# Kernel optimization log

Measured on AMD Instinct MI355X. Metric: run time of the kernel, lower is better.

The kernel has to match this reference:

```python
import jax, jax.numpy as jnp
import numpy as np

D_MODEL = 1024
H = 16
D_K = D_MODEL // H
BAND = 100  # attention allowed where |i-j| < BAND


def setup_inputs() -> dict:
    key = jax.random.key(0)
    ks = jax.random.split(key, 9)
    B, S = 2, 2048
    s = 1.0 / np.sqrt(D_MODEL)
    return {
        "x": jax.random.normal(ks[0], (B, S, D_MODEL), jnp.float32),
        "Wq": jax.random.normal(ks[1], (D_MODEL, D_MODEL), jnp.float32) * s,
        "bq": jnp.zeros((D_MODEL,), jnp.float32),
        "Wk": jax.random.normal(ks[2], (D_MODEL, D_MODEL), jnp.float32) * s,
        "bk": jnp.zeros((D_MODEL,), jnp.float32),
        "Wv": jax.random.normal(ks[3], (D_MODEL, D_MODEL), jnp.float32) * s,
        "bv": jnp.zeros((D_MODEL,), jnp.float32),
        "Wo": jax.random.normal(ks[4], (D_MODEL, D_MODEL), jnp.float32) * s,
        "bo": jnp.zeros((D_MODEL,), jnp.float32),
    }


def _split_heads(t, B, S):
    # [B, S, D] -> [B, H, S, D_K]
    return t.reshape(B, S, H, D_K).transpose(0, 2, 1, 3)


def reference(x, Wq, bq, Wk, bk, Wv, bv, Wo, bo):
    B, S, _ = x.shape
    q = _split_heads(x @ Wq.T + bq, B, S)
    k = _split_heads(x @ Wk.T + bk, B, S)
    v = _split_heads(x @ Wv.T + bv, B, S)

    scores = jnp.einsum("bhqd,bhkd->bhqk", q, k) / jnp.sqrt(jnp.float32(D_K))
    i = jnp.arange(S)
    band = jnp.abs(i[:, None] - i[None, :]) < BAND  # [S, S] True inside band
    scores = jnp.where(band[None, None, :, :], scores, jnp.float32(-1e9))
    p_attn = jax.nn.softmax(scores, axis=-1)

    out = jnp.einsum("bhqk,bhkd->bhqd", p_attn, v)
    out = out.transpose(0, 2, 1, 3).reshape(B, S, D_MODEL)
    return out @ Wo.T + bo
```

## Files before the change

### kernel.cpp

```cpp
#include <hip/hip_runtime.h>
#include <hip/hip_bf16.h>


typedef __attribute__((ext_vector_type(8))) short short8;
typedef __attribute__((ext_vector_type(4))) short short4v;
typedef __attribute__((ext_vector_type(4))) float f32x4;

#define S_LEN 2048
#define NH 16
#define DK 64
#define BANDW 100

#define X_ELEMS   (2 * S_LEN * 1024)
#define W_ELEMS   (1024 * 1024)
#define QKV_ELEMS (2 * NH * S_LEN * DK)
#define AO_ELEMS  (2 * S_LEN * 1024)

__device__ __attribute__((aligned(256))) short g_X[X_ELEMS];
__device__ __attribute__((aligned(256))) short g_W[4 * W_ELEMS];
__device__ __attribute__((aligned(256))) short g_b[4 * 1024];
__device__ __attribute__((aligned(256))) short g_Q[QKV_ELEMS];
__device__ __attribute__((aligned(256))) short g_K[QKV_ELEMS];
__device__ __attribute__((aligned(256))) short g_V[QKV_ELEMS];
__device__ __attribute__((aligned(256))) short g_AO[AO_ELEMS];

__device__ __forceinline__ float bf2f(short u) {
    unsigned x = ((unsigned)(unsigned short)u) << 16;
    return __builtin_bit_cast(float, x);
}
__device__ __forceinline__ short f2bf(float f) {
    unsigned x = __builtin_bit_cast(unsigned, f);
    unsigned r = (x + 0x7fffu + ((x >> 16) & 1u)) >> 16;
    return (short)r;
}

#define GLOAD_LDS(gp, lp) \
    __builtin_amdgcn_global_load_lds( \
        (const __attribute__((address_space(1))) void*)(gp), \
        (__attribute__((address_space(3))) void*)(lp), 16, 0, 0)

#define XC   (X_ELEMS / 8)
#define WC   (W_ELEMS / 8)
#define BC   (1024 / 8)
#define TOTC (XC + 4 * WC + 4 * BC)

__global__ __launch_bounds__(256) void convert_all(
    const void* __restrict__ x,
    const void* __restrict__ w0, const void* __restrict__ b0,
    const void* __restrict__ w1, const void* __restrict__ b1,
    const void* __restrict__ w2, const void* __restrict__ b2,
    const void* __restrict__ w3, const void* __restrict__ b3)
{
    __shared__ int cnt[256];
    {
        const unsigned* xw = (const unsigned*)x;
        int local = 0;
        #pragma unroll
        for (int i = 0; i < 4; i++) {
            unsigned wv = xw[threadIdx.x * 4 + i];
            unsigned e = (wv >> 7) & 0xFF;
            if (e >= 100 && e <= 140) local++;
        }
        cnt[threadIdx.x] = local;
    }
    __syncthreads();
    for (int s = 128; s > 0; s >>= 1) {
        if (threadIdx.x < s) cnt[threadIdx.x] += cnt[threadIdx.x + s];
        __syncthreads();
    }
    const int is_bf16 = (cnt[0] > 512);

    long i = (long)blockIdx.x * 256 + threadIdx.x;
    if (i >= TOTC) return;

    const void* src; short* dst; long off;
    if (i < XC)                { src = x;  dst = g_X;              off = i; }
    else if ((i -= XC) < WC)   { src = w0; dst = g_W + 0L*W_ELEMS; off = i; }
    else if ((i -= WC) < WC)   { src = w1; dst = g_W + 1L*W_ELEMS; off = i; }
    else if ((i -= WC) < WC)   { src = w2; dst = g_W + 2L*W_ELEMS; off = i; }
    else if ((i -= WC) < WC)   { src = w3; dst = g_W + 3L*W_ELEMS; off = i; }
    else if ((i -= WC) < BC)   { src = b0; dst = g_b + 0*1024;     off = i; }
    else if ((i -= BC) < BC)   { src = b1; dst = g_b + 1*1024;     off = i; }
    else if ((i -= BC) < BC)   { src = b2; dst = g_b + 2*1024;     off = i; }
    else                       { src = b3; dst = g_b + 3*1024;     off = i - BC; }

    if (is_bf16) {
        ((short8*)dst)[off] = ((const short8*)src)[off];
    } else {
        const float* s = (const float*)src + off * 8;
        short8 o;
        #pragma unroll
        for (int e = 0; e < 8; e++) o[e] = f2bf(s[e]);
        ((short8*)dst)[off] = o;
    }
}

__global__ __launch_bounds__(256) void qkv_gemm()
{
    __shared__ __attribute__((aligned(16))) short As[128 * 32];
    __shared__ __attribute__((aligned(16))) short Bs[128 * 32];

    const int z = blockIdx.z;
    const short* __restrict__ X = g_X;
    const short* __restrict__ W = g_W + (long)z * W_ELEMS;
    const short* __restrict__ bias = g_b + z * 1024;

    const int t = threadIdx.x;
    const int lane = t & 63;
    const int wid  = t >> 6;
    const int wm = wid & 1, wn = wid >> 1;
    const int l15 = lane & 15;
    const int q8  = (lane >> 4) * 8;
    const int mb = blockIdx.x * 128;
    const int nb = blockIdx.y * 128;

    const long ga0 = (long)(mb + (t >> 2)) * 1024 + (t & 3) * 8;
    const long ga1 = (long)(mb + 64 + (t >> 2)) * 1024 + (t & 3) * 8;
    const long gb0 = (long)(nb + (t >> 2)) * 1024 + (t & 3) * 8;
    const long gb1 = (long)(nb + 64 + (t >> 2)) * 1024 + (t & 3) * 8;
    short* lA0 = As + t * 8;
    short* lA1 = As + 2048 + t * 8;
    short* lB0 = Bs + t * 8;
    short* lB1 = Bs + 2048 + t * 8;

    f32x4 acc[4][4] = {};

    for (int k0 = 0; k0 < 1024; k0 += 32) {
        __syncthreads();
        GLOAD_LDS(X + ga0 + k0, lA0);
        GLOAD_LDS(X + ga1 + k0, lA1);
        GLOAD_LDS(W + gb0 + k0, lB0);
        GLOAD_LDS(W + gb1 + k0, lB1);
        __syncthreads();

        short8 a[4], b[4];
        #pragma unroll
        for (int mt = 0; mt < 4; mt++) a[mt] = *(const short8*)(As + (wm * 64 + mt * 16 + l15) * 32 + q8);
        #pragma unroll
        for (int nt = 0; nt < 4; nt++) b[nt] = *(const short8*)(Bs + (wn * 64 + nt * 16 + l15) * 32 + q8);
        #pragma unroll
        for (int mt = 0; mt < 4; mt++)
            #pragma unroll
            for (int nt = 0; nt < 4; nt++)
                acc[mt][nt] = __builtin_amdgcn_mfma_f32_16x16x32_bf16(a[mt], b[nt], acc[mt][nt], 0, 0, 0);
    }

    const int rg = (lane >> 4) * 4;
    if (z == 2) {
        #pragma unroll
        for (int nt = 0; nt < 4; nt++) {
            const int col = nb + wn * 64 + nt * 16 + l15;
            const float bv_ = bf2f(bias[col]);
            const int h = col >> 6, d = col & 63;
            #pragma unroll
            for (int mt = 0; mt < 4; mt++) {
                const int row0 = mb + wm * 64 + mt * 16 + rg;
                const int bI = row0 >> 11, s0 = row0 & 2047;
                short4v pk;
                #pragma unroll
                for (int r = 0; r < 4; r++) pk[r] = f2bf(acc[mt][nt][r] + bv_);
                *(short4v*)(g_V + (((long)(bI * NH + h) * DK) + d) * S_LEN + s0) = pk;
            }
        }
    } else {
        short* __restrict__ Out = (z == 0) ? g_Q : g_K;
        #pragma unroll
        for (int nt = 0; nt < 4; nt++) {
            const int col = nb + wn * 64 + nt * 16 + l15;
            const float bv_ = bf2f(bias[col]);
            const int h = col >> 6, d = col & 63;
            #pragma unroll
            for (int mt = 0; mt < 4; mt++) {
                #pragma unroll
                for (int r = 0; r < 4; r++) {
                    const int row = mb + wm * 64 + mt * 16 + rg + r;
                    const int bI = row >> 11, s = row & 2047;
                    Out[(((long)(bI * NH + h) * S_LEN) + s) * DK + d] = f2bf(acc[mt][nt][r] + bv_);
                }
            }
        }
    }
}

__global__ __launch_bounds__(256) void o_gemm(float* __restrict__ Out)
{
    __shared__ __attribute__((aligned(16))) short As[128 * 32];
    __shared__ __attribute__((aligned(16))) short Bs[64 * 32];

    const short* __restrict__ A = g_AO;
    const short* __restrict__ W = g_W + 3L * W_ELEMS;

    const int t = threadIdx.x;
    const int lane = t & 63;
    const int wid  = t >> 6;
    const int wm = wid & 1, wn = wid >> 1;
    const int l15 = lane & 15;
    const int q8  = (lane >> 4) * 8;
    const int mb = blockIdx.x * 128;
    const int nb = blockIdx.y * 64;

    const long ga0 = (long)(mb + (t >> 2)) * 1024 + (t & 3) * 8;
    const long ga1 = (long)(mb + 64 + (t >> 2)) * 1024 + (t & 3) * 8;
    const long gb0 = (long)(nb + (t >> 2)) * 1024 + (t & 3) * 8;
    short* lA0 = As + t * 8;
    short* lA1 = As + 2048 + t * 8;
    short* lB0 = Bs + t * 8;

    f32x4 acc[4][2] = {};

    for (int k0 = 0; k0 < 1024; k0 += 32) {
        __syncthreads();
        GLOAD_LDS(A + ga0 + k0, lA0);
        GLOAD_LDS(A + ga1 + k0, lA1);
        GLOAD_LDS(W + gb0 + k0, lB0);
        __syncthreads();

        short8 a[4], b[2];
        #pragma unroll
        for (int mt = 0; mt < 4; mt++) a[mt] = *(const short8*)(As + (wm * 64 + mt * 16 + l15) * 32 + q8);
        #pragma unroll
        for (int nt = 0; nt < 2; nt++) b[nt] = *(const short8*)(Bs + (wn * 32 + nt * 16 + l15) * 32 + q8);
        #pragma unroll
        for (int mt = 0; mt < 4; mt++)
            #pragma unroll
            for (int nt = 0; nt < 2; nt++)
                acc[mt][nt] = __builtin_amdgcn_mfma_f32_16x16x32_bf16(a[mt], b[nt], acc[mt][nt], 0, 0, 0);
    }

    const int rg = (lane >> 4) * 4;
    #pragma unroll
    for (int nt = 0; nt < 2; nt++) {
        const int col = nb + wn * 32 + nt * 16 + l15;
        const float bv_ = bf2f(g_b[3 * 1024 + col]);
        #pragma unroll
        for (int mt = 0; mt < 4; mt++) {
            #pragma unroll
            for (int r = 0; r < 4; r++) {
                const int row = mb + wm * 64 + mt * 16 + rg + r;
                Out[(long)row * 1024 + col] = acc[mt][nt][r] + bv_;
            }
        }
    }
}

__global__ __launch_bounds__(256) void attn_kernel()
{
    __shared__ __attribute__((aligned(16))) short Pl[4][16][72];

    const int bid = blockIdx.x;
    const int qt = bid & 31;
    const int h  = (bid >> 5) & 15;
    const int b  = bid >> 9;
    const int qbase = qt * 64;

    const int lane = threadIdx.x & 63;
    const int w    = threadIdx.x >> 6;
    const int l15  = lane & 15;
    const int qg   = lane >> 4;
    const int q8   = qg * 8;

    const long hoff = (long)(b * NH + h) * S_LEN * DK;
    const short* __restrict__ Qh = g_Q + hoff;
    const short* __restrict__ Kh = g_K + hoff;
    const short* __restrict__ Vt = g_V + hoff;

    const short* qp = Qh + (long)(qbase + w * 16 + l15) * DK + q8;
    const short8 aq0 = *(const short8*)(qp);
    const short8 aq1 = *(const short8*)(qp + 32);

    f32x4 o[4] = {};
    float m_r[4], l_r[4];
    #pragma unroll
    for (int r = 0; r < 4; r++) { m_r[r] = -1e30f; l_r[r] = 0.f; }

    const int lo  = qbase - (BANDW - 1);
    const int kc0 = (lo < 0 ? 0 : lo) >> 6;
    int hi = qbase + 64 + (BANDW - 1);
    if (hi > S_LEN) hi = S_LEN;
    const int kc1 = (hi + 63) >> 6;

    for (int kc = kc0; kc < kc1; kc++) {
        const int kb = kc * 64;

        f32x4 sc[4];
        #pragma unroll
        for (int nt = 0; nt < 4; nt++) {
            const short* kp = Kh + (long)(kb + nt * 16 + l15) * DK + q8;
            const short8 bk0 = *(const short8*)(kp);
            const short8 bk1 = *(const short8*)(kp + 32);
            f32x4 z = {};
            z = __builtin_amdgcn_mfma_f32_16x16x32_bf16(aq0, bk0, z, 0, 0, 0);
            z = __builtin_amdgcn_mfma_f32_16x16x32_bf16(aq1, bk1, z, 0, 0, 0);
            sc[nt] = z;
        }

        float pv[4][4];
        float mx[4] = {-1e30f, -1e30f, -1e30f, -1e30f};
        #pragma unroll
        for (int nt = 0; nt < 4; nt++) {
            const int kg = kb + nt * 16 + l15;
            #pragma unroll
            for (int r = 0; r < 4; r++) {
                const int qI = qbase + w * 16 + qg * 4 + r;
                int dlt = qI - kg; if (dlt < 0) dlt = -dlt;
                const float v = (dlt < BANDW) ? sc[nt][r] * 0.125f : -1e30f;
                pv[nt][r] = v;
                mx[r] = fmaxf(mx[r], v);
            }
        }
        #pragma unroll
        for (int mk = 1; mk < 16; mk <<= 1)
            #pragma unroll
            for (int r = 0; r < 4; r++) mx[r] = fmaxf(mx[r], __shfl_xor(mx[r], mk, 64));

        float alpha[4], lnew[4];
        #pragma unroll
        for (int r = 0; r < 4; r++) {
            const float mn = fmaxf(m_r[r], mx[r]);
            alpha[r] = __builtin_exp2f((m_r[r] - mn) * 1.44269504f);
            m_r[r] = mn;
            lnew[r] = 0.f;
        }
        #pragma unroll
        for (int nt = 0; nt < 4; nt++)
            #pragma unroll
            for (int r = 0; r < 4; r++) {
                const float p = (pv[nt][r] > -0.5e30f)
                    ? __builtin_exp2f((pv[nt][r] - m_r[r]) * 1.44269504f) : 0.f;
                pv[nt][r] = p;
                lnew[r] += p;
            }
        #pragma unroll
        for (int mk = 1; mk < 16; mk <<= 1)
            #pragma unroll
            for (int r = 0; r < 4; r++) lnew[r] += __shfl_xor(lnew[r], mk, 64);
        #pragma unroll
        for (int r = 0; r < 4; r++) l_r[r] = l_r[r] * alpha[r] + lnew[r];
        #pragma unroll
        for (int nt2 = 0; nt2 < 4; nt2++)
            #pragma unroll
            for (int r = 0; r < 4; r++) o[nt2][r] *= alpha[r];

        #pragma unroll
        for (int nt = 0; nt < 4; nt++)
            #pragma unroll
            for (int r = 0; r < 4; r++)
                Pl[w][qg * 4 + r][nt * 16 + l15] = f2bf(pv[nt][r]);
        asm volatile("s_waitcnt lgkmcnt(0)" ::: "memory");
        const short8 ap0 = *(const short8*)(&Pl[w][l15][q8]);
        const short8 ap1 = *(const short8*)(&Pl[w][l15][32 + q8]);

        #pragma unroll
        for (int nt2 = 0; nt2 < 4; nt2++) {
            const short* vp = Vt + (long)(nt2 * 16 + l15) * S_LEN + kb;
            const short8 bv0 = *(const short8*)(vp + q8);
            const short8 bv1 = *(const short8*)(vp + 32 + q8);
            o[nt2] = __builtin_amdgcn_mfma_f32_16x16x32_bf16(ap0, bv0, o[nt2], 0, 0, 0);
            o[nt2] = __builtin_amdgcn_mfma_f32_16x16x32_bf16(ap1, bv1, o[nt2], 0, 0, 0);
        }
    }

    #pragma unroll
    for (int nt2 = 0; nt2 < 4; nt2++)
        #pragma unroll
        for (int r = 0; r < 4; r++) {
            const int qI = qbase + w * 16 + qg * 4 + r;
            const int d = nt2 * 16 + l15;
            g_AO[((long)b * S_LEN + qI) * 1024 + h * DK + d] = f2bf(o[nt2][r] / l_r[r]);
        }
}

extern "C" void kernel_launch(void* const* d_in, const int* in_sizes, int n_in,
                              void* d_out, int out_size, void* d_ws, size_t ws_size,
                              hipStream_t stream) {
    float* out = (float*)d_out;

    convert_all<<<(TOTC + 255) / 256, 256, 0, stream>>>(
        d_in[0], d_in[1], d_in[2], d_in[3], d_in[4], d_in[5], d_in[6], d_in[7], d_in[8]);
    qkv_gemm<<<dim3(32, 8, 3), 256, 0, stream>>>();
    attn_kernel<<<dim3(2 * NH * (S_LEN / 64)), 256, 0, stream>>>();
    o_gemm<<<dim3(32, 16), 256, 0, stream>>>(out);
}
```

Before: 198.1 us.

## Store V row-major and transpose it into shared memory inside attention

The QKV GEMM now writes V in the same [B,H,S,D] row-major layout as Q and K, dropping the special transposed store path. The attention kernel loads the band's V rows once per block, transposes them into a padded shared-memory tile, and reads the MFMA B operands from LDS instead of global memory. The intent is to replace strided global writes and repeated global V reads with one cooperative load per block. In exchange it adds a scalar-scatter LDS transpose, a barrier and about 41 KB of shared memory per block, which may cost bank conflicts and occupancy.

```diff
diff --git a/kernel.cpp b/kernel.cpp
--- a/kernel.cpp
+++ b/kernel.cpp
@@ -3,7 +3,6 @@
 
 
 typedef __attribute__((ext_vector_type(8))) short short8;
-typedef __attribute__((ext_vector_type(4))) short short4v;
 typedef __attribute__((ext_vector_type(4))) float f32x4;
 
 #define S_LEN 2048
@@ -104,6 +103,7 @@
     const short* __restrict__ X = g_X;
     const short* __restrict__ W = g_W + (long)z * W_ELEMS;
     const short* __restrict__ bias = g_b + z * 1024;
+    short* __restrict__ Out = (z == 0) ? g_Q : ((z == 1) ? g_K : g_V);
 
     const int t = threadIdx.x;
     const int lane = t & 63;
@@ -146,37 +146,18 @@
     }
 
     const int rg = (lane >> 4) * 4;
-    if (z == 2) {
-        #pragma unroll
-        for (int nt = 0; nt < 4; nt++) {
-            const int col = nb + wn * 64 + nt * 16 + l15;
-            const float bv_ = bf2f(bias[col]);
-            const int h = col >> 6, d = col & 63;
-            #pragma unroll
-            for (int mt = 0; mt < 4; mt++) {
-                const int row0 = mb + wm * 64 + mt * 16 + rg;
-                const int bI = row0 >> 11, s0 = row0 & 2047;
-                short4v pk;
-                #pragma unroll
-                for (int r = 0; r < 4; r++) pk[r] = f2bf(acc[mt][nt][r] + bv_);
-                *(short4v*)(g_V + (((long)(bI * NH + h) * DK) + d) * S_LEN + s0) = pk;
-            }
-        }
-    } else {
-        short* __restrict__ Out = (z == 0) ? g_Q : g_K;
-        #pragma unroll
-        for (int nt = 0; nt < 4; nt++) {
-            const int col = nb + wn * 64 + nt * 16 + l15;
-            const float bv_ = bf2f(bias[col]);
-            const int h = col >> 6, d = col & 63;
-            #pragma unroll
-            for (int mt = 0; mt < 4; mt++) {
-                #pragma unroll
-                for (int r = 0; r < 4; r++) {
-                    const int row = mb + wm * 64 + mt * 16 + rg + r;
-                    const int bI = row >> 11, s = row & 2047;
-                    Out[(((long)(bI * NH + h) * S_LEN) + s) * DK + d] = f2bf(acc[mt][nt][r] + bv_);
-                }
+    #pragma unroll
+    for (int nt = 0; nt < 4; nt++) {
+        const int col = nb + wn * 64 + nt * 16 + l15;
+        const float bv_ = bf2f(bias[col]);
+        const int h = col >> 6, d = col & 63;
+        #pragma unroll
+        for (int mt = 0; mt < 4; mt++) {
+            #pragma unroll
+            for (int r = 0; r < 4; r++) {
+                const int row = mb + wm * 64 + mt * 16 + rg + r;
+                const int bI = row >> 11, s = row & 2047;
+                Out[(((long)(bI * NH + h) * S_LEN) + s) * DK + d] = f2bf(acc[mt][nt][r] + bv_);
             }
         }
     }
@@ -243,8 +224,11 @@
     }
 }
 
+#define VT_PAD 328
+
 __global__ __launch_bounds__(256) void attn_kernel()
 {
+    __shared__ __attribute__((aligned(16))) short Vt[64][VT_PAD];
     __shared__ __attribute__((aligned(16))) short Pl[4][16][72];
 
     const int bid = blockIdx.x;
@@ -262,25 +246,39 @@
     const long hoff = (long)(b * NH + h) * S_LEN * DK;
     const short* __restrict__ Qh = g_Q + hoff;
     const short* __restrict__ Kh = g_K + hoff;
-    const short* __restrict__ Vt = g_V + hoff;
-
-    const short* qp = Qh + (long)(qbase + w * 16 + l15) * DK + q8;
-    const short8 aq0 = *(const short8*)(qp);
-    const short8 aq1 = *(const short8*)(qp + 32);
-
-    f32x4 o[4] = {};
-    float m_r[4], l_r[4];
-    #pragma unroll
-    for (int r = 0; r < 4; r++) { m_r[r] = -1e30f; l_r[r] = 0.f; }
+    const short* __restrict__ Vh = g_V + hoff;
 
     const int lo  = qbase - (BANDW - 1);
     const int kc0 = (lo < 0 ? 0 : lo) >> 6;
     int hi = qbase + 64 + (BANDW - 1);
     if (hi > S_LEN) hi = S_LEN;
     const int kc1 = (hi + 63) >> 6;
+    const int kb0 = kc0 * 64;
+    const int n_keys = (kc1 - kc0) * 64;
+
+    const short* qp = Qh + (long)(qbase + w * 16 + l15) * DK + q8;
+    const short8 aq0 = *(const short8*)(qp);
+    const short8 aq1 = *(const short8*)(qp + 32);
+
+    for (int kk = threadIdx.x; kk < n_keys; kk += 256) {
+        const short* vp = Vh + (long)(kb0 + kk) * DK;
+        #pragma unroll
+        for (int tq = 0; tq < 8; tq++) {
+            const short8 v = *(const short8*)(vp + tq * 8);
+            #pragma unroll
+            for (int e = 0; e < 8; e++) Vt[tq * 8 + e][kk] = v[e];
+        }
+    }
+    __syncthreads();
+
+    f32x4 o[4] = {};
+    float m_r[4], l_r[4];
+    #pragma unroll
+    for (int r = 0; r < 4; r++) { m_r[r] = -1e30f; l_r[r] = 0.f; }
 
     for (int kc = kc0; kc < kc1; kc++) {
         const int kb = kc * 64;
+        const int kloc = kb - kb0;
 
         f32x4 sc[4];
         #pragma unroll
@@ -352,9 +350,9 @@
 
         #pragma unroll
         for (int nt2 = 0; nt2 < 4; nt2++) {
-            const short* vp = Vt + (long)(nt2 * 16 + l15) * S_LEN + kb;
-            const short8 bv0 = *(const short8*)(vp + q8);
-            const short8 bv1 = *(const short8*)(vp + 32 + q8);
+            const short* vrow = &Vt[nt2 * 16 + l15][kloc];
+            const short8 bv0 = *(const short8*)(vrow + q8);
+            const short8 bv1 = *(const short8*)(vrow + 32 + q8);
             o[nt2] = __builtin_amdgcn_mfma_f32_16x16x32_bf16(ap0, bv0, o[nt2], 0, 0, 0);
             o[nt2] = __builtin_amdgcn_mfma_f32_16x16x32_bf16(ap1, bv1, o[nt2], 0, 0, 0);
         }
```

New measurement: 179.0 us. 9.7% less time.
